# Performance work log

Measured on AMD Instinct MI355X. Metric: run time of the kernel, lower is better.

Reference implementation:

```python
import jax, jax.numpy as jnp
import numpy as np

# Llama-7B-like decode-step config (GQA)
H = 32      # query heads
HKV = 8     # kv heads
D = 128     # head dim
HID = 4096  # hidden size (= H*D)
S = 32768   # stored quantized cache length
B = 1       # batch
Q = 1       # q_len (fused SmartKV path requires q_len == 1)


def rotate_half(x):
    return jnp.concatenate([-x[..., D // 2:], x[..., :D // 2]], axis=-1)


def setup_inputs() -> dict:
    key = jax.random.key(0)
    ks = jax.random.split(key, 9)
    hidden_states = jax.random.normal(ks[0], (B, Q, HID), jnp.float32)
    # quantized KV cache: signed int codes + per-(token, kv_head) scales
    k_qx = jax.random.randint(ks[1], (S, HKV, D), -128, 128, jnp.int32)
    v_qx = jax.random.randint(ks[2], (S, HKV, D), -128, 128, jnp.int32)
    k_scale = jax.random.uniform(ks[3], (S, HKV, 1), jnp.float32, 0.005, 0.02)
    v_scale = jax.random.uniform(ks[4], (S, HKV, 1), jnp.float32, 0.005, 0.02)
    # RoPE angles for the current decode position (pos = S)
    inv_freq = 1.0 / (10000.0 ** (jnp.arange(0, D, 2).astype(jnp.float32) / D))
    ang = jnp.concatenate([S * inv_freq, S * inv_freq])  # [D]
    cos = jnp.cos(ang)
    sin = jnp.sin(ang)
    sc = 1.0 / np.sqrt(HID)
    Wq = jax.random.normal(ks[5], (HID, H * D), jnp.float32) * sc
    Wk = jax.random.normal(ks[6], (HID, HKV * D), jnp.float32) * sc
    Wv = jax.random.normal(ks[7], (HID, HKV * D), jnp.float32) * sc
    Wo = jax.random.normal(ks[8], (H * D, HID), jnp.float32) * sc
    return dict(hidden_states=hidden_states, k_qx=k_qx, k_scale=k_scale,
                v_qx=v_qx, v_scale=v_scale, cos=cos, sin=sin,
                Wq=Wq, Wk=Wk, Wv=Wv, Wo=Wo)


def reference(hidden_states, k_qx, k_scale, v_qx, v_scale, cos, sin, Wq, Wk, Wv, Wo):
    b, q_len, _ = hidden_states.shape  # b=1, q_len=1 (decode)
    G = H // HKV  # GQA group size
    # QKV projections
    q = (hidden_states @ Wq).reshape(b, q_len, H, D).transpose(0, 2, 1, 3)      # [B,H,Q,D]
    k = (hidden_states @ Wk).reshape(b, q_len, HKV, D).transpose(0, 2, 1, 3)    # [B,HKV,Q,D]
    v = (hidden_states @ Wv).reshape(b, q_len, HKV, D).transpose(0, 2, 1, 3)    # [B,HKV,Q,D]
    # RoPE on current-token q, k
    c = cos[None, None, None, :]
    s = sin[None, None, None, :]
    q = q * c + rotate_half(q) * s
    k = k * c + rotate_half(k) * s
    # inline dequantization of SmartKV cache (kept at HKV heads; GQA handled in einsum
    # instead of materializing repeat_interleave)
    Kp = k_qx.astype(jnp.float32) * k_scale  # [S,HKV,D]
    Vp = v_qx.astype(jnp.float32) * v_scale  # [S,HKV,D]
    qg = q.reshape(b, HKV, G, q_len, D)
    scale = 1.0 / jnp.sqrt(jnp.float32(D))
    s_past = jnp.einsum('bkgqd,skd->bkgqs', qg, Kp) * scale        # [B,HKV,G,Q,S]
    s_cur = jnp.einsum('bkgqd,bkqd->bkgq', qg, k)[..., None] * scale  # current token
    scores = jnp.concatenate([s_past, s_cur], axis=-1)             # [B,HKV,G,Q,S+1]
    probs = jax.nn.softmax(scores, axis=-1)
    out = (jnp.einsum('bkgqs,skd->bkgqd', probs[..., :S], Vp)
           + probs[..., S:] * v[:, :, None, :, :])                 # [B,HKV,G,Q,D]
    out = out.reshape(b, H, q_len, D).transpose(0, 2, 1, 3).reshape(b, q_len, H * D)
    return out @ Wo
```

## Files before the change

### kernel.cpp

```cpp
#include <hip/hip_runtime.h>
#include <hip/hip_bf16.h>

#define H_    32
#define HKV_  8
#define D_    128
#define HID_  4096
#define NQKV  6144
#define SPLIT 128
#define CHUNK 256
#define TB    16
#define NT    (CHUNK / TB)
#define S_    32768
#define NCHUNK (S_ / CHUNK)
#define SCALE_ 0.08838834764831843f
#define BASE_  8.0f

#define GLOAD_LDS16(g, l) __builtin_amdgcn_global_load_lds( \
    (const __attribute__((address_space(1))) void*)(g),     \
    (__attribute__((address_space(3))) void*)(l), 16, 0, 0)
#define GLOAD_LDS4(g, l) __builtin_amdgcn_global_load_lds(  \
    (const __attribute__((address_space(1))) void*)(g),     \
    (__attribute__((address_space(3))) void*)(l), 4, 0, 0)

#define WS_QKV_PART 0
#define WS_QKV      786432
#define WS_PV_C     792576
#define WS_L_C      1316864
#define WS_ATTN     1320960
#define WS_OPART    1325056

__global__ __launch_bounds__(256) void k_qkv_part(
    const float* __restrict__ hid, const float* __restrict__ Wq,
    const float* __restrict__ Wk, const float* __restrict__ Wv,
    float* __restrict__ part)
{
    const int j0 = blockIdx.x * 1024 + threadIdx.x * 4;
    const int i0 = blockIdx.y * (HID_ / SPLIT);
    __shared__ float hs[HID_ / SPLIT];
    if (threadIdx.x < HID_ / SPLIT) hs[threadIdx.x] = hid[i0 + threadIdx.x];
    __syncthreads();

    const float* W; int ldw; int col;
    if (j0 < 4096)       { W = Wq; ldw = 4096; col = j0; }
    else if (j0 < 5120)  { W = Wk; ldw = 1024; col = j0 - 4096; }
    else                 { W = Wv; ldw = 1024; col = j0 - 5120; }

    float4 acc = {0.f, 0.f, 0.f, 0.f};
    const float* p = W + (size_t)i0 * ldw + col;
    #pragma unroll 8
    for (int i = 0; i < HID_ / SPLIT; ++i) {
        const float4 wv = *(const float4*)(p + (size_t)i * ldw);
        const float h = hs[i];
        acc.x += h * wv.x; acc.y += h * wv.y; acc.z += h * wv.z; acc.w += h * wv.w;
    }
    *(float4*)&part[(size_t)blockIdx.y * NQKV + j0] = acc;
}

__global__ __launch_bounds__(256) void k_qkv_reduce(
    const float* __restrict__ part, const float* __restrict__ cosv,
    const float* __restrict__ sinv, float* __restrict__ qkv)
{
    const int j = blockIdx.x * 256 + threadIdx.x;
    float s = 0.f;
    #pragma unroll 8
    for (int k = 0; k < SPLIT; ++k) s += part[(size_t)k * NQKV + j];
    __shared__ float buf[256];
    buf[threadIdx.x] = s;
    __syncthreads();
    float out = s;
    if (j < 5120) {
        const int d = j & 127;
        const float rot = (d < 64) ? -buf[threadIdx.x + 64] : buf[threadIdx.x - 64];
        out = s * cosv[d] + rot * sinv[d];
    }
    qkv[j] = out;
}

__global__ __launch_bounds__(256) void k_attn(
    const int* __restrict__ kqx, const float* __restrict__ kscale,
    const int* __restrict__ vqx, const float* __restrict__ vscale,
    const float* __restrict__ qkv, float* __restrict__ pv_c,
    float* __restrict__ l_c)
{
    const int kh = blockIdx.y;
    const int c0 = blockIdx.x * CHUNK;
    const int tid = threadIdx.x;
    const int g = tid >> 6;
    const int l = tid & 63;
    const int t = l >> 3, j = l & 7;

    __shared__ int   kbuf[2][TB * 128];
    __shared__ int   vbuf[2][TB * 128];
    __shared__ float scbuf[2][64];

    float4 qf[4];
    #pragma unroll
    for (int k = 0; k < 4; ++k)
        qf[k] = *(const float4*)&qkv[(kh * 4 + g) * D_ + (j + 8 * k) * 4];

    float ls = 0.f;
    float4 acc[4];
    #pragma unroll
    for (int k = 0; k < 4; ++k) acc[k] = make_float4(0.f, 0.f, 0.f, 0.f);

    auto stage = [&](int buf, int tok0) {
        #pragma unroll
        for (int i = 0; i < 2; ++i) {
            const int seg = g * 4 + i * 2;
            const int row = seg + (l >> 5);
            const int col = ((l & 31) * 16) ^ ((row & 3) << 7);
            const size_t goff = ((size_t)(tok0 + row) * HKV_ + kh) * D_ + (col >> 2);
            GLOAD_LDS16(kqx + goff, (char*)&kbuf[buf][0] + seg * 512);
            GLOAD_LDS16(vqx + goff, (char*)&vbuf[buf][0] + seg * 512);
        }
        if (g == 0) {
            const float* gs;
            if (l < 16)      gs = kscale + (size_t)(tok0 + l) * HKV_ + kh;
            else if (l < 32) gs = vscale + (size_t)(tok0 + (l - 16)) * HKV_ + kh;
            else             gs = kscale + (size_t)tok0 * HKV_ + kh;
            GLOAD_LDS4(gs, (char*)&scbuf[buf][0]);
        }
    };

    stage(0, c0);
    __syncthreads();

    for (int tile = 0; tile < NT; ++tile) {
        if (tile + 1 < NT) stage((tile + 1) & 1, c0 + (tile + 1) * TB);

        const int buf = tile & 1;
        #pragma unroll
        for (int it = 0; it < TB / 8; ++it) {
            const int row = it * 8 + t;
            const int sw = (row & 3) << 7;
            int4 kv[4], vv[4];
            #pragma unroll
            for (int k = 0; k < 4; ++k) {
                const int off = row * 512 + (((j + 8 * k) * 16) ^ sw);
                kv[k] = *(const int4*)((const char*)&kbuf[buf][0] + off);
                vv[k] = *(const int4*)((const char*)&vbuf[buf][0] + off);
            }
            const float sc = scbuf[buf][row] * SCALE_;
            const float vs = scbuf[buf][16 + row];

            float dot = 0.f;
            #pragma unroll
            for (int k = 0; k < 4; ++k)
                dot += (float)kv[k].x * qf[k].x + (float)kv[k].y * qf[k].y +
                       (float)kv[k].z * qf[k].z + (float)kv[k].w * qf[k].w;
            dot += __shfl_xor(dot, 1, 64);
            dot += __shfl_xor(dot, 2, 64);
            dot += __shfl_xor(dot, 4, 64);

            const float wgt = __expf(dot * sc - BASE_);
            ls += wgt;
            const float wv = wgt * vs;
            #pragma unroll
            for (int k = 0; k < 4; ++k) {
                acc[k].x += wv * (float)vv[k].x;
                acc[k].y += wv * (float)vv[k].y;
                acc[k].z += wv * (float)vv[k].z;
                acc[k].w += wv * (float)vv[k].w;
            }
        }
        __syncthreads();
    }

    #pragma unroll
    for (int msk = 8; msk < 64; msk <<= 1) {
        #pragma unroll
        for (int k = 0; k < 4; ++k) {
            acc[k].x += __shfl_xor(acc[k].x, msk, 64);
            acc[k].y += __shfl_xor(acc[k].y, msk, 64);
            acc[k].z += __shfl_xor(acc[k].z, msk, 64);
            acc[k].w += __shfl_xor(acc[k].w, msk, 64);
        }
        ls += __shfl_xor(ls, msk, 64);
    }
    if (t == 0) {
        float* dst = pv_c + ((size_t)(blockIdx.x * HKV_ + kh) * 4 + g) * D_;
        #pragma unroll
        for (int k = 0; k < 4; ++k) *(float4*)(dst + (j + 8 * k) * 4) = acc[k];
        if (j == 0) l_c[(blockIdx.x * HKV_ + kh) * 4 + g] = ls;
    }
}

__global__ __launch_bounds__(128) void k_combine(
    const float* __restrict__ pv_c, const float* __restrict__ l_c,
    const float* __restrict__ qkv, float* __restrict__ attn)
{
    const int h = blockIdx.x;
    const int d = threadIdx.x;
    const int kh = h >> 2, g = h & 3;

    __shared__ float sred[128];
    sred[d] = qkv[h * D_ + d] * qkv[4096 + kh * D_ + d];
    __syncthreads();
    for (int s2 = 64; s2 > 0; s2 >>= 1) {
        if (d < s2) sred[d] += sred[d + s2];
        __syncthreads();
    }
    const float pc = __expf(sred[0] * SCALE_ - BASE_);

    float pv = 0.f, dsum = 0.f;
    for (int c = 0; c < NCHUNK; ++c) {
        pv   += pv_c[((size_t)(c * HKV_ + kh) * 4 + g) * D_ + d];
        dsum += l_c[(c * HKV_ + kh) * 4 + g];
    }
    const float vcur = qkv[5120 + kh * D_ + d];
    attn[h * D_ + d] = (pv + pc * vcur) / (dsum + pc);
}

__global__ __launch_bounds__(256) void k_out_part(
    const float* __restrict__ attn, const float* __restrict__ Wo,
    float* __restrict__ opart)
{
    const int j0 = blockIdx.x * 1024 + threadIdx.x * 4;
    const int i0 = blockIdx.y * (HID_ / SPLIT);
    __shared__ float hs[HID_ / SPLIT];
    if (threadIdx.x < HID_ / SPLIT) hs[threadIdx.x] = attn[i0 + threadIdx.x];
    __syncthreads();
    float4 acc = {0.f, 0.f, 0.f, 0.f};
    const float* p = Wo + (size_t)i0 * HID_ + j0;
    #pragma unroll 8
    for (int i = 0; i < HID_ / SPLIT; ++i) {
        const float4 wv = *(const float4*)(p + (size_t)i * HID_);
        const float h = hs[i];
        acc.x += h * wv.x; acc.y += h * wv.y; acc.z += h * wv.z; acc.w += h * wv.w;
    }
    *(float4*)&opart[(size_t)blockIdx.y * HID_ + j0] = acc;
}

__global__ __launch_bounds__(256) void k_out_reduce(
    const float* __restrict__ opart, float* __restrict__ out)
{
    const int j = blockIdx.x * 256 + threadIdx.x;
    float s = 0.f;
    #pragma unroll 8
    for (int k = 0; k < SPLIT; ++k) s += opart[(size_t)k * HID_ + j];
    out[j] = s;
}

extern "C" void kernel_launch(void* const* d_in, const int* in_sizes, int n_in,
                              void* d_out, int out_size, void* d_ws, size_t ws_size,
                              hipStream_t stream) {
    const float* hid    = (const float*)d_in[0];
    const int*   kqx    = (const int*)d_in[1];
    const float* kscale = (const float*)d_in[2];
    const int*   vqx    = (const int*)d_in[3];
    const float* vscale = (const float*)d_in[4];
    const float* cosv   = (const float*)d_in[5];
    const float* sinv   = (const float*)d_in[6];
    const float* Wq     = (const float*)d_in[7];
    const float* Wk     = (const float*)d_in[8];
    const float* Wv     = (const float*)d_in[9];
    const float* Wo     = (const float*)d_in[10];
    float* ws  = (float*)d_ws;
    float* out = (float*)d_out;

    k_qkv_part  <<<dim3(6, SPLIT), 256, 0, stream>>>(hid, Wq, Wk, Wv, ws + WS_QKV_PART);
    k_qkv_reduce<<<dim3(24),       256, 0, stream>>>(ws + WS_QKV_PART, cosv, sinv, ws + WS_QKV);
    k_attn      <<<dim3(NCHUNK, HKV_), 256, 0, stream>>>(kqx, kscale, vqx, vscale,
                                                         ws + WS_QKV, ws + WS_PV_C,
                                                         ws + WS_L_C);
    k_combine   <<<dim3(H_),       128, 0, stream>>>(ws + WS_PV_C, ws + WS_L_C,
                                                     ws + WS_QKV, ws + WS_ATTN);
    k_out_part  <<<dim3(4, SPLIT), 256, 0, stream>>>(ws + WS_ATTN, Wo, ws + WS_OPART);
    k_out_reduce<<<dim3(16),       256, 0, stream>>>(ws + WS_OPART, out);
}
```

Before: 120.3 us.

## Triple-buffer KV tiles with vmcnt waits and per-wave scale buffers

Switches the attention kernel's LDS staging from double to triple buffering, prefetching two tiles ahead. The __syncthreads pair is replaced by an explicit s_waitcnt vmcnt plus a raw s_barrier, so more async global-to-LDS loads stay in flight. Each wave now loads its own copy of the scales, which lets it wait only on its own vmcnt. The dot product is split into four independent partial sums to shorten the dependency chain. In exchange it uses more LDS, which may lower occupancy. The hand-counted vmcnt value is fragile if the number of issued loads changes.

```diff
diff --git a/kernel.cpp b/kernel.cpp
--- a/kernel.cpp
+++ b/kernel.cpp
@@ -21,6 +21,7 @@
 #define GLOAD_LDS4(g, l) __builtin_amdgcn_global_load_lds(  \
     (const __attribute__((address_space(1))) void*)(g),     \
     (__attribute__((address_space(3))) void*)(l), 4, 0, 0)
+#define WAITV(N) asm volatile("s_waitcnt vmcnt(" #N ")" ::: "memory")
 
 #define WS_QKV_PART 0
 #define WS_QKV      786432
@@ -89,9 +90,9 @@
     const int l = tid & 63;
     const int t = l >> 3, j = l & 7;
 
-    __shared__ int   kbuf[2][TB * 128];
-    __shared__ int   vbuf[2][TB * 128];
-    __shared__ float scbuf[2][64];
+    __shared__ int   kbuf[3][TB * 128];
+    __shared__ int   vbuf[3][TB * 128];
+    __shared__ float scbuf[3][4][64];
 
     float4 qf[4];
     #pragma unroll
@@ -113,22 +114,25 @@
             GLOAD_LDS16(kqx + goff, (char*)&kbuf[buf][0] + seg * 512);
             GLOAD_LDS16(vqx + goff, (char*)&vbuf[buf][0] + seg * 512);
         }
-        if (g == 0) {
+        {
             const float* gs;
             if (l < 16)      gs = kscale + (size_t)(tok0 + l) * HKV_ + kh;
             else if (l < 32) gs = vscale + (size_t)(tok0 + (l - 16)) * HKV_ + kh;
             else             gs = kscale + (size_t)tok0 * HKV_ + kh;
-            GLOAD_LDS4(gs, (char*)&scbuf[buf][0]);
+            GLOAD_LDS4(gs, (char*)&scbuf[buf][g][0]);
         }
     };
 
     stage(0, c0);
-    __syncthreads();
+    stage(1, c0 + TB);
 
     for (int tile = 0; tile < NT; ++tile) {
-        if (tile + 1 < NT) stage((tile + 1) & 1, c0 + (tile + 1) * TB);
-
-        const int buf = tile & 1;
+        if (tile + 1 < NT) { WAITV(5); } else { WAITV(0); }
+        __builtin_amdgcn_s_barrier();
+        __builtin_amdgcn_sched_barrier(0);
+        if (tile + 2 < NT) stage((tile + 2) % 3, c0 + (tile + 2) * TB);
+
+        const int buf = tile % 3;
         #pragma unroll
         for (int it = 0; it < TB / 8; ++it) {
             const int row = it * 8 + t;
@@ -140,14 +144,19 @@
                 kv[k] = *(const int4*)((const char*)&kbuf[buf][0] + off);
                 vv[k] = *(const int4*)((const char*)&vbuf[buf][0] + off);
             }
-            const float sc = scbuf[buf][row] * SCALE_;
-            const float vs = scbuf[buf][16 + row];
-
-            float dot = 0.f;
-            #pragma unroll
-            for (int k = 0; k < 4; ++k)
-                dot += (float)kv[k].x * qf[k].x + (float)kv[k].y * qf[k].y +
-                       (float)kv[k].z * qf[k].z + (float)kv[k].w * qf[k].w;
+            const float sc = scbuf[buf][g][row] * SCALE_;
+            const float vs = scbuf[buf][g][16 + row];
+
+            float d0 = 0.f, d1 = 0.f, d2 = 0.f, d3 = 0.f;
+            d0 += (float)kv[0].x * qf[0].x + (float)kv[0].y * qf[0].y +
+                  (float)kv[0].z * qf[0].z + (float)kv[0].w * qf[0].w;
+            d1 += (float)kv[1].x * qf[1].x + (float)kv[1].y * qf[1].y +
+                  (float)kv[1].z * qf[1].z + (float)kv[1].w * qf[1].w;
+            d2 += (float)kv[2].x * qf[2].x + (float)kv[2].y * qf[2].y +
+                  (float)kv[2].z * qf[2].z + (float)kv[2].w * qf[2].w;
+            d3 += (float)kv[3].x * qf[3].x + (float)kv[3].y * qf[3].y +
+                  (float)kv[3].z * qf[3].z + (float)kv[3].w * qf[3].w;
+            float dot = (d0 + d1) + (d2 + d3);
             dot += __shfl_xor(dot, 1, 64);
             dot += __shfl_xor(dot, 2, 64);
             dot += __shfl_xor(dot, 4, 64);
@@ -163,7 +172,6 @@
                 acc[k].w += wv * (float)vv[k].w;
             }
         }
-        __syncthreads();
     }
 
     #pragma unroll
```

Result: slower. 138.4 us (+15.1%).

## Double attention block threads, splitting tile rows across two half-blocks with LDS merge

Applied to the files above, without the earlier changes.

The attention kernel now runs 512 threads per block. Each group of four waves processes half of the 16 tokens in every staged tile, and each wave issues one row-pair of async global-to-LDS loads instead of two. The two halves' partial PV accumulators and softmax denominators are merged through shared memory before the write-out. The intent is more memory-level parallelism and latency hiding on the bandwidth-bound KV stream, at the cost of a larger block, an extra sync and merge, and possibly lower occupancy per CU. The combine loop also gets an unroll hint.

```diff
diff --git a/kernel.cpp b/kernel.cpp
--- a/kernel.cpp
+++ b/kernel.cpp
@@ -76,7 +76,7 @@
     qkv[j] = out;
 }
 
-__global__ __launch_bounds__(256) void k_attn(
+__global__ __launch_bounds__(512) void k_attn(
     const int* __restrict__ kqx, const float* __restrict__ kscale,
     const int* __restrict__ vqx, const float* __restrict__ vscale,
     const float* __restrict__ qkv, float* __restrict__ pv_c,
@@ -85,13 +85,16 @@
     const int kh = blockIdx.y;
     const int c0 = blockIdx.x * CHUNK;
     const int tid = threadIdx.x;
-    const int g = tid >> 6;
+    const int w = tid >> 6;
+    const int g = w & 3;
+    const int hh = w >> 2;
     const int l = tid & 63;
     const int t = l >> 3, j = l & 7;
 
     __shared__ int   kbuf[2][TB * 128];
     __shared__ int   vbuf[2][TB * 128];
     __shared__ float scbuf[2][64];
+    __shared__ float merge[4][8][17];
 
     float4 qf[4];
     #pragma unroll
@@ -104,16 +107,12 @@
     for (int k = 0; k < 4; ++k) acc[k] = make_float4(0.f, 0.f, 0.f, 0.f);
 
     auto stage = [&](int buf, int tok0) {
-        #pragma unroll
-        for (int i = 0; i < 2; ++i) {
-            const int seg = g * 4 + i * 2;
-            const int row = seg + (l >> 5);
-            const int col = ((l & 31) * 16) ^ ((row & 3) << 7);
-            const size_t goff = ((size_t)(tok0 + row) * HKV_ + kh) * D_ + (col >> 2);
-            GLOAD_LDS16(kqx + goff, (char*)&kbuf[buf][0] + seg * 512);
-            GLOAD_LDS16(vqx + goff, (char*)&vbuf[buf][0] + seg * 512);
-        }
-        if (g == 0) {
+        const int row = 2 * w + (l >> 5);
+        const int col = ((l & 31) * 16) ^ ((row & 3) << 7);
+        const size_t goff = ((size_t)(tok0 + row) * HKV_ + kh) * D_ + (col >> 2);
+        GLOAD_LDS16(kqx + goff, (char*)&kbuf[buf][0] + w * 1024);
+        GLOAD_LDS16(vqx + goff, (char*)&vbuf[buf][0] + w * 1024);
+        if (w == 0) {
             const float* gs;
             if (l < 16)      gs = kscale + (size_t)(tok0 + l) * HKV_ + kh;
             else if (l < 32) gs = vscale + (size_t)(tok0 + (l - 16)) * HKV_ + kh;
@@ -129,39 +128,41 @@
         if (tile + 1 < NT) stage((tile + 1) & 1, c0 + (tile + 1) * TB);
 
         const int buf = tile & 1;
-        #pragma unroll
-        for (int it = 0; it < TB / 8; ++it) {
-            const int row = it * 8 + t;
-            const int sw = (row & 3) << 7;
-            int4 kv[4], vv[4];
-            #pragma unroll
-            for (int k = 0; k < 4; ++k) {
-                const int off = row * 512 + (((j + 8 * k) * 16) ^ sw);
-                kv[k] = *(const int4*)((const char*)&kbuf[buf][0] + off);
-                vv[k] = *(const int4*)((const char*)&vbuf[buf][0] + off);
-            }
-            const float sc = scbuf[buf][row] * SCALE_;
-            const float vs = scbuf[buf][16 + row];
-
-            float dot = 0.f;
-            #pragma unroll
-            for (int k = 0; k < 4; ++k)
-                dot += (float)kv[k].x * qf[k].x + (float)kv[k].y * qf[k].y +
-                       (float)kv[k].z * qf[k].z + (float)kv[k].w * qf[k].w;
-            dot += __shfl_xor(dot, 1, 64);
-            dot += __shfl_xor(dot, 2, 64);
-            dot += __shfl_xor(dot, 4, 64);
-
-            const float wgt = __expf(dot * sc - BASE_);
-            ls += wgt;
-            const float wv = wgt * vs;
-            #pragma unroll
-            for (int k = 0; k < 4; ++k) {
-                acc[k].x += wv * (float)vv[k].x;
-                acc[k].y += wv * (float)vv[k].y;
-                acc[k].z += wv * (float)vv[k].z;
-                acc[k].w += wv * (float)vv[k].w;
-            }
+        const int row = hh * 8 + t;
+        const int sw = (row & 3) << 7;
+        int4 kv[4], vv[4];
+        #pragma unroll
+        for (int k = 0; k < 4; ++k) {
+            const int off = row * 512 + (((j + 8 * k) * 16) ^ sw);
+            kv[k] = *(const int4*)((const char*)&kbuf[buf][0] + off);
+            vv[k] = *(const int4*)((const char*)&vbuf[buf][0] + off);
+        }
+        const float sc = scbuf[buf][row] * SCALE_;
+        const float vs = scbuf[buf][16 + row];
+
+        float d0 = 0.f, d1 = 0.f, d2 = 0.f, d3 = 0.f;
+        d0 += (float)kv[0].x * qf[0].x + (float)kv[0].y * qf[0].y +
+              (float)kv[0].z * qf[0].z + (float)kv[0].w * qf[0].w;
+        d1 += (float)kv[1].x * qf[1].x + (float)kv[1].y * qf[1].y +
+              (float)kv[1].z * qf[1].z + (float)kv[1].w * qf[1].w;
+        d2 += (float)kv[2].x * qf[2].x + (float)kv[2].y * qf[2].y +
+              (float)kv[2].z * qf[2].z + (float)kv[2].w * qf[2].w;
+        d3 += (float)kv[3].x * qf[3].x + (float)kv[3].y * qf[3].y +
+              (float)kv[3].z * qf[3].z + (float)kv[3].w * qf[3].w;
+        float dot = (d0 + d1) + (d2 + d3);
+        dot += __shfl_xor(dot, 1, 64);
+        dot += __shfl_xor(dot, 2, 64);
+        dot += __shfl_xor(dot, 4, 64);
+
+        const float wgt = __expf(dot * sc - BASE_);
+        ls += wgt;
+        const float wv = wgt * vs;
+        #pragma unroll
+        for (int k = 0; k < 4; ++k) {
+            acc[k].x += wv * (float)vv[k].x;
+            acc[k].y += wv * (float)vv[k].y;
+            acc[k].z += wv * (float)vv[k].z;
+            acc[k].w += wv * (float)vv[k].w;
         }
         __syncthreads();
     }
@@ -177,7 +178,19 @@
         }
         ls += __shfl_xor(ls, msk, 64);
     }
-    if (t == 0) {
+    if (hh == 1 && t == 0) {
+        #pragma unroll
+        for (int k = 0; k < 4; ++k) *(float4*)&merge[g][j][k * 4] = acc[k];
+        merge[g][j][16] = ls;
+    }
+    __syncthreads();
+    if (hh == 0 && t == 0) {
+        #pragma unroll
+        for (int k = 0; k < 4; ++k) {
+            const float4 m = *(const float4*)&merge[g][j][k * 4];
+            acc[k].x += m.x; acc[k].y += m.y; acc[k].z += m.z; acc[k].w += m.w;
+        }
+        ls += merge[g][j][16];
         float* dst = pv_c + ((size_t)(blockIdx.x * HKV_ + kh) * 4 + g) * D_;
         #pragma unroll
         for (int k = 0; k < 4; ++k) *(float4*)(dst + (j + 8 * k) * 4) = acc[k];
@@ -203,6 +216,7 @@
     const float pc = __expf(sred[0] * SCALE_ - BASE_);
 
     float pv = 0.f, dsum = 0.f;
+    #pragma unroll 4
     for (int c = 0; c < NCHUNK; ++c) {
         pv   += pv_c[((size_t)(c * HKV_ + kh) * 4 + g) * D_ + d];
         dsum += l_c[(c * HKV_ + kh) * 4 + g];
@@ -260,7 +274,7 @@
 
     k_qkv_part  <<<dim3(6, SPLIT), 256, 0, stream>>>(hid, Wq, Wk, Wv, ws + WS_QKV_PART);
     k_qkv_reduce<<<dim3(24),       256, 0, stream>>>(ws + WS_QKV_PART, cosv, sinv, ws + WS_QKV);
-    k_attn      <<<dim3(NCHUNK, HKV_), 256, 0, stream>>>(kqx, kscale, vqx, vscale,
+    k_attn      <<<dim3(NCHUNK, HKV_), 512, 0, stream>>>(kqx, kscale, vqx, vscale,
                                                          ws + WS_QKV, ws + WS_PV_C,
                                                          ws + WS_L_C);
     k_combine   <<<dim3(H_),       128, 0, stream>>>(ws + WS_PV_C, ws + WS_L_C,
```

New measurement: 121.5 us. About the same (+1.0%).

## Process all KV heads per attention block with GQA group reuse of K/V

Applied to the files above, without the earlier changes.

The attention kernel is restructured so each 512-thread block covers one 64-token chunk across all 8 KV heads, with one wave per KV head. Each lane now computes scores for all 4 query heads of its GQA group, so one loaded K/V element serves four heads. Staging copies whole contiguous token rows (all heads) into LDS. The trade-off is four times as many chunk partials, which makes the combine kernel's serial reduction longer, plus a block-wide sync after every 4-token tile.

```diff
diff --git a/kernel.cpp b/kernel.cpp
--- a/kernel.cpp
+++ b/kernel.cpp
@@ -7,8 +7,8 @@
 #define HID_  4096
 #define NQKV  6144
 #define SPLIT 128
-#define CHUNK 256
-#define TB    16
+#define CHUNK 64
+#define TB    4
 #define NT    (CHUNK / TB)
 #define S_    32768
 #define NCHUNK (S_ / CHUNK)
@@ -22,12 +22,12 @@
     (const __attribute__((address_space(1))) void*)(g),     \
     (__attribute__((address_space(3))) void*)(l), 4, 0, 0)
 
+#define WS_PV_C     0
 #define WS_QKV_PART 0
-#define WS_QKV      786432
-#define WS_PV_C     792576
-#define WS_L_C      1316864
-#define WS_ATTN     1320960
-#define WS_OPART    1325056
+#define WS_QKV      2097152
+#define WS_L_C      2103296
+#define WS_ATTN     2119680
+#define WS_OPART    2123776
 
 __global__ __launch_bounds__(256) void k_qkv_part(
     const float* __restrict__ hid, const float* __restrict__ Wq,
@@ -76,112 +76,125 @@
     qkv[j] = out;
 }
 
-__global__ __launch_bounds__(256) void k_attn(
+__global__ __launch_bounds__(512) void k_attn(
     const int* __restrict__ kqx, const float* __restrict__ kscale,
     const int* __restrict__ vqx, const float* __restrict__ vscale,
     const float* __restrict__ qkv, float* __restrict__ pv_c,
     float* __restrict__ l_c)
 {
-    const int kh = blockIdx.y;
-    const int c0 = blockIdx.x * CHUNK;
+    const int c = blockIdx.x;
+    const int tok0b = c * CHUNK;
     const int tid = threadIdx.x;
-    const int g = tid >> 6;
+    const int w = tid >> 6;
     const int l = tid & 63;
-    const int t = l >> 3, j = l & 7;
-
-    __shared__ int   kbuf[2][TB * 128];
-    __shared__ int   vbuf[2][TB * 128];
-    __shared__ float scbuf[2][64];
-
-    float4 qf[4];
+    const int t = l >> 4, jj = l & 15;
+
+    __shared__ int   kbuf[2][TB * HKV_ * 128];
+    __shared__ int   vbuf[2][TB * HKV_ * 128];
+    __shared__ float scb[2][64];
+
+    float4 qfa[4], qfb[4];
     #pragma unroll
-    for (int k = 0; k < 4; ++k)
-        qf[k] = *(const float4*)&qkv[(kh * 4 + g) * D_ + (j + 8 * k) * 4];
-
-    float ls = 0.f;
-    float4 acc[4];
+    for (int g = 0; g < 4; ++g) {
+        qfa[g] = *(const float4*)&qkv[(w * 4 + g) * D_ + jj * 4];
+        qfb[g] = *(const float4*)&qkv[(w * 4 + g) * D_ + 64 + jj * 4];
+    }
+
+    float ls[4] = {0.f, 0.f, 0.f, 0.f};
+    float4 accA[4], accB[4];
     #pragma unroll
-    for (int k = 0; k < 4; ++k) acc[k] = make_float4(0.f, 0.f, 0.f, 0.f);
+    for (int g = 0; g < 4; ++g) {
+        accA[g] = make_float4(0.f, 0.f, 0.f, 0.f);
+        accB[g] = make_float4(0.f, 0.f, 0.f, 0.f);
+    }
 
     auto stage = [&](int buf, int tok0) {
         #pragma unroll
         for (int i = 0; i < 2; ++i) {
-            const int seg = g * 4 + i * 2;
-            const int row = seg + (l >> 5);
-            const int col = ((l & 31) * 16) ^ ((row & 3) << 7);
-            const size_t goff = ((size_t)(tok0 + row) * HKV_ + kh) * D_ + (col >> 2);
-            GLOAD_LDS16(kqx + goff, (char*)&kbuf[buf][0] + seg * 512);
-            GLOAD_LDS16(vqx + goff, (char*)&vbuf[buf][0] + seg * 512);
-        }
-        if (g == 0) {
-            const float* gs;
-            if (l < 16)      gs = kscale + (size_t)(tok0 + l) * HKV_ + kh;
-            else if (l < 32) gs = vscale + (size_t)(tok0 + (l - 16)) * HKV_ + kh;
-            else             gs = kscale + (size_t)tok0 * HKV_ + kh;
-            GLOAD_LDS4(gs, (char*)&scbuf[buf][0]);
+            const int seg = w * 2 + i;
+            const size_t src = (size_t)tok0 * 1024 + seg * 256 + l * 4;
+            GLOAD_LDS16(kqx + src, (char*)&kbuf[buf][0] + seg * 1024);
+            GLOAD_LDS16(vqx + src, (char*)&vbuf[buf][0] + seg * 1024);
+        }
+        if (w == 0) {
+            const float* gs = (l < 32) ? (kscale + (size_t)tok0 * HKV_ + l)
+                                       : (vscale + (size_t)tok0 * HKV_ + (l - 32));
+            GLOAD_LDS4(gs, (char*)&scb[buf][0]);
         }
     };
 
-    stage(0, c0);
+    stage(0, tok0b);
     __syncthreads();
 
     for (int tile = 0; tile < NT; ++tile) {
-        if (tile + 1 < NT) stage((tile + 1) & 1, c0 + (tile + 1) * TB);
+        if (tile + 1 < NT) stage((tile + 1) & 1, tok0b + (tile + 1) * TB);
 
         const int buf = tile & 1;
-        #pragma unroll
-        for (int it = 0; it < TB / 8; ++it) {
-            const int row = it * 8 + t;
-            const int sw = (row & 3) << 7;
-            int4 kv[4], vv[4];
+        const int base = t * 1024 + w * 128;
+        const int4 kA = *(const int4*)&kbuf[buf][base + jj * 4];
+        const int4 kB = *(const int4*)&kbuf[buf][base + 64 + jj * 4];
+        const int4 vA = *(const int4*)&vbuf[buf][base + jj * 4];
+        const int4 vB = *(const int4*)&vbuf[buf][base + 64 + jj * 4];
+        const float ksc = scb[buf][t * 8 + w] * SCALE_;
+        const float vsc = scb[buf][32 + t * 8 + w];
+
+        const float a0 = (float)kA.x, a1 = (float)kA.y, a2 = (float)kA.z, a3 = (float)kA.w;
+        const float b0 = (float)kB.x, b1 = (float)kB.y, b2 = (float)kB.z, b3 = (float)kB.w;
+        float dot[4];
+        #pragma unroll
+        for (int g = 0; g < 4; ++g)
+            dot[g] = a0 * qfa[g].x + a1 * qfa[g].y + a2 * qfa[g].z + a3 * qfa[g].w +
+                     b0 * qfb[g].x + b1 * qfb[g].y + b2 * qfb[g].z + b3 * qfb[g].w;
+        #pragma unroll
+        for (int msk = 1; msk < 16; msk <<= 1) {
             #pragma unroll
-            for (int k = 0; k < 4; ++k) {
-                const int off = row * 512 + (((j + 8 * k) * 16) ^ sw);
-                kv[k] = *(const int4*)((const char*)&kbuf[buf][0] + off);
-                vv[k] = *(const int4*)((const char*)&vbuf[buf][0] + off);
-            }
-            const float sc = scbuf[buf][row] * SCALE_;
-            const float vs = scbuf[buf][16 + row];
-
-            float dot = 0.f;
+            for (int g = 0; g < 4; ++g) dot[g] += __shfl_xor(dot[g], msk, 64);
+        }
+        float wv[4];
+        #pragma unroll
+        for (int g = 0; g < 4; ++g) {
+            const float wgt = __expf(dot[g] * ksc - BASE_);
+            ls[g] += wgt;
+            wv[g] = wgt * vsc;
+        }
+        const float c0f = (float)vA.x, c1f = (float)vA.y, c2f = (float)vA.z, c3f = (float)vA.w;
+        const float d0f = (float)vB.x, d1f = (float)vB.y, d2f = (float)vB.z, d3f = (float)vB.w;
+        #pragma unroll
+        for (int g = 0; g < 4; ++g) {
+            accA[g].x += wv[g] * c0f; accA[g].y += wv[g] * c1f;
+            accA[g].z += wv[g] * c2f; accA[g].w += wv[g] * c3f;
+            accB[g].x += wv[g] * d0f; accB[g].y += wv[g] * d1f;
+            accB[g].z += wv[g] * d2f; accB[g].w += wv[g] * d3f;
+        }
+        __syncthreads();
+    }
+
+    #pragma unroll
+    for (int msk = 16; msk < 64; msk <<= 1) {
+        #pragma unroll
+        for (int g = 0; g < 4; ++g) {
+            accA[g].x += __shfl_xor(accA[g].x, msk, 64);
+            accA[g].y += __shfl_xor(accA[g].y, msk, 64);
+            accA[g].z += __shfl_xor(accA[g].z, msk, 64);
+            accA[g].w += __shfl_xor(accA[g].w, msk, 64);
+            accB[g].x += __shfl_xor(accB[g].x, msk, 64);
+            accB[g].y += __shfl_xor(accB[g].y, msk, 64);
+            accB[g].z += __shfl_xor(accB[g].z, msk, 64);
+            accB[g].w += __shfl_xor(accB[g].w, msk, 64);
+            ls[g] += __shfl_xor(ls[g], msk, 64);
+        }
+    }
+    if (t == 0) {
+        #pragma unroll
+        for (int g = 0; g < 4; ++g) {
+            float* dst = pv_c + (((size_t)c * HKV_ + w) * 4 + g) * D_;
+            *(float4*)(dst + jj * 4) = accA[g];
+            *(float4*)(dst + 64 + jj * 4) = accB[g];
+        }
+        if (jj == 0) {
             #pragma unroll
-            for (int k = 0; k < 4; ++k)
-                dot += (float)kv[k].x * qf[k].x + (float)kv[k].y * qf[k].y +
-                       (float)kv[k].z * qf[k].z + (float)kv[k].w * qf[k].w;
-            dot += __shfl_xor(dot, 1, 64);
-            dot += __shfl_xor(dot, 2, 64);
-            dot += __shfl_xor(dot, 4, 64);
-
-            const float wgt = __expf(dot * sc - BASE_);
-            ls += wgt;
-            const float wv = wgt * vs;
-            #pragma unroll
-            for (int k = 0; k < 4; ++k) {
-                acc[k].x += wv * (float)vv[k].x;
-                acc[k].y += wv * (float)vv[k].y;
-                acc[k].z += wv * (float)vv[k].z;
-                acc[k].w += wv * (float)vv[k].w;
-            }
-        }
-        __syncthreads();
-    }
-
-    #pragma unroll
-    for (int msk = 8; msk < 64; msk <<= 1) {
-        #pragma unroll
-        for (int k = 0; k < 4; ++k) {
-            acc[k].x += __shfl_xor(acc[k].x, msk, 64);
-            acc[k].y += __shfl_xor(acc[k].y, msk, 64);
-            acc[k].z += __shfl_xor(acc[k].z, msk, 64);
-            acc[k].w += __shfl_xor(acc[k].w, msk, 64);
-        }
-        ls += __shfl_xor(ls, msk, 64);
-    }
-    if (t == 0) {
-        float* dst = pv_c + ((size_t)(blockIdx.x * HKV_ + kh) * 4 + g) * D_;
-        #pragma unroll
-        for (int k = 0; k < 4; ++k) *(float4*)(dst + (j + 8 * k) * 4) = acc[k];
-        if (j == 0) l_c[(blockIdx.x * HKV_ + kh) * 4 + g] = ls;
+            for (int g = 0; g < 4; ++g) l_c[((size_t)c * HKV_ + w) * 4 + g] = ls[g];
+        }
     }
 }
 
@@ -203,9 +216,10 @@
     const float pc = __expf(sred[0] * SCALE_ - BASE_);
 
     float pv = 0.f, dsum = 0.f;
+    #pragma unroll 4
     for (int c = 0; c < NCHUNK; ++c) {
-        pv   += pv_c[((size_t)(c * HKV_ + kh) * 4 + g) * D_ + d];
-        dsum += l_c[(c * HKV_ + kh) * 4 + g];
+        pv   += pv_c[(((size_t)c * HKV_ + kh) * 4 + g) * D_ + d];
+        dsum += l_c[((size_t)c * HKV_ + kh) * 4 + g];
     }
     const float vcur = qkv[5120 + kh * D_ + d];
     attn[h * D_ + d] = (pv + pc * vcur) / (dsum + pc);
@@ -260,9 +274,9 @@
 
     k_qkv_part  <<<dim3(6, SPLIT), 256, 0, stream>>>(hid, Wq, Wk, Wv, ws + WS_QKV_PART);
     k_qkv_reduce<<<dim3(24),       256, 0, stream>>>(ws + WS_QKV_PART, cosv, sinv, ws + WS_QKV);
-    k_attn      <<<dim3(NCHUNK, HKV_), 256, 0, stream>>>(kqx, kscale, vqx, vscale,
-                                                         ws + WS_QKV, ws + WS_PV_C,
-                                                         ws + WS_L_C);
+    k_attn      <<<dim3(NCHUNK),   512, 0, stream>>>(kqx, kscale, vqx, vscale,
+                                                     ws + WS_QKV, ws + WS_PV_C,
+                                                     ws + WS_L_C);
     k_combine   <<<dim3(H_),       128, 0, stream>>>(ws + WS_PV_C, ws + WS_L_C,
                                                      ws + WS_QKV, ws + WS_ATTN);
     k_out_part  <<<dim3(4, SPLIT), 256, 0, stream>>>(ws + WS_ATTN, Wo, ws + WS_OPART);
```

Result: slower. 149.8 us (+24.5%).
